# Optimization experiments

Hardware: AMD Instinct MI355X
Metric: run time of the kernel (lower is better)

The kernel has to match this reference:

```python
import jax, jax.numpy as jnp
import numpy as np


def _rel_shift(x):
    # Transformer-XL relative shift. x: [batch, heads, qlen, klen]
    b, n, i, j = x.shape
    x = jnp.pad(x, ((0, 0), (0, 0), (0, 0), (1, 0)))  # zero-pad along key axis
    x = x.reshape(b, n, j + 1, i)[:, :, 1:, :]
    return x.reshape(b, n, i, j)


def setup_inputs() -> dict:
    key = jax.random.key(0)
    ks = jax.random.split(key, 7)
    QLEN, B, D, H, DH = 2048, 4, 1024, 16, 64
    DO = H * DH
    s = 1.0 / np.sqrt(D)
    return {
        "word_embed": jax.random.normal(ks[0], (QLEN, B, D), jnp.float32),
        "pos_embed": jax.random.normal(ks[1], (QLEN, D), jnp.float32),
        "bias_q": jax.random.normal(ks[2], (H, DH), jnp.float32) * 0.02,
        "bias_k": jax.random.normal(ks[3], (H, DH), jnp.float32) * 0.02,
        "W_qkv": jax.random.normal(ks[4], (D, 3 * DO), jnp.float32) * s,
        "W_r": jax.random.normal(ks[5], (D, DO), jnp.float32) * s,
        "b_r": jnp.zeros((DO,), jnp.float32),
    }


def reference(word_embed, pos_embed, bias_q, bias_k, W_qkv, W_r, b_r):
    qlen, bsz, dim = word_embed.shape
    H, Dh = bias_q.shape
    plen = pos_embed.shape[0]

    # fused QKV projection (no bias, as in torch Linear(bias=False))
    qkv = jnp.einsum('ibd,de->ibe', word_embed, W_qkv)  # [qlen, b, 3*H*Dh]
    q, k, v = jnp.split(qkv, 3, axis=-1)
    q = q.reshape(qlen, bsz, H, Dh)
    k = k.reshape(qlen, bsz, H, Dh)
    v = v.reshape(qlen, bsz, H, Dh)

    # positional projection (r_net has bias)
    r = (pos_embed @ W_r + b_r).reshape(plen, H, Dh)  # [plen, H, Dh]

    # content (AC) and position (BD) score terms
    AC = jnp.einsum('ibnd,jbnd->bnij', q + bias_q, k)   # [b, H, qlen, klen]
    BD = jnp.einsum('ibnd,jnd->bnij', q + bias_k, r)    # [b, H, qlen, plen]
    BD = _rel_shift(BD)

    scale = float(Dh) ** 0.5
    attn = jax.nn.softmax((AC + BD) / scale, axis=-1)
    ctx = jnp.einsum('bnij,jbnd->ibnd', attn, v)        # [qlen, b, H, Dh]
    return ctx.reshape(qlen, bsz, H * Dh)
```

## Files before the change

kernel.cpp:

```cpp
#include <hip/hip_runtime.h>
#include <stdint.h>

typedef unsigned short u16;
typedef __attribute__((ext_vector_type(8))) short  s16x8;
typedef __attribute__((ext_vector_type(8))) __bf16 b16x8;
typedef __attribute__((ext_vector_type(4))) float  f32x4;

__device__ __forceinline__ float bf2f(u16 u){
  union { unsigned int ui; float f; } v; v.ui = ((unsigned int)u) << 16; return v.f;
}
__device__ __forceinline__ u16 f2bf(float f){
  union { float f; unsigned int ui; } v; v.f = f;
  unsigned int u = v.ui;
  u += 0x7FFFu + ((u >> 16) & 1u);
  return (u16)(u >> 16);
}
__device__ __forceinline__ f32x4 mfma16(s16x8 a, s16x8 b, f32x4 c){
  return __builtin_amdgcn_mfma_f32_16x16x32_bf16(
      __builtin_bit_cast(b16x8, a), __builtin_bit_cast(b16x8, b), c, 0, 0, 0);
}
__device__ __forceinline__ void gload_lds16(const u16* g, u16* l){
  __builtin_amdgcn_global_load_lds(
      (const __attribute__((address_space(1))) unsigned int*)(g),
      (__attribute__((address_space(3))) unsigned int*)(l), 16, 0, 0);
}

__global__ __launch_bounds__(256) void cast_f32_bf16(const float* __restrict__ in,
                                                     u16* __restrict__ out, int n8){
  int i = blockIdx.x * 256 + threadIdx.x;
  if (i >= n8) return;
  const f32x4* p = (const f32x4*)(in + (size_t)i * 8);
  f32x4 a = p[0], c = p[1];
  s16x8 o;
#pragma unroll
  for (int j = 0; j < 4; j++){ o[j] = (short)f2bf(a[j]); o[j+4] = (short)f2bf(c[j]); }
  *(s16x8*)(out + (size_t)i * 8) = o;
}

__global__ __launch_bounds__(256) void tcast(const float* __restrict__ in,
                                             u16* __restrict__ out, int R, int C){
  __shared__ float tile[32][33];
  int c0 = blockIdx.x * 32, r0 = blockIdx.y * 32;
  int tc = threadIdx.x & 31, tr = threadIdx.x >> 5;
#pragma unroll
  for (int p = 0; p < 4; p++)
    tile[tr + 8*p][tc] = in[(size_t)(r0 + tr + 8*p) * C + c0 + tc];
  __syncthreads();
  int rr = threadIdx.x & 31, cc = threadIdx.x >> 5;
#pragma unroll
  for (int p = 0; p < 4; p++)
    out[(size_t)(c0 + cc + 8*p) * R + r0 + rr] = f2bf(tile[rr][cc + 8*p]);
}

__global__ __launch_bounds__(256) void gemm_bt(const u16* __restrict__ A,
                                               const u16* __restrict__ Bt,
                                               int mode,
                                               u16* __restrict__ Qo, u16* __restrict__ Ko,
                                               u16* __restrict__ Vo, u16* __restrict__ Ro,
                                               const float* __restrict__ brp){
  __shared__ __align__(16) u16 lsA[2][128 * 32];
  __shared__ __align__(16) u16 lsB[2][128 * 32];
  int m0 = blockIdx.y * 128, n0 = blockIdx.x * 128;
  int t = threadIdx.x, wid = t >> 6, lane = t & 63;
  int lrow = lane & 15, lk = lane >> 4;
  int wr = wid >> 1, wc = wid & 1;

  f32x4 acc[4][4];
#pragma unroll
  for (int i = 0; i < 4; i++)
#pragma unroll
    for (int j = 0; j < 4; j++) acc[i][j] = (f32x4){0.f, 0.f, 0.f, 0.f};

  const u16* Ab = A  + (size_t)m0 * 1024;
  const u16* Bb = Bt + (size_t)n0 * 1024;

  s16x8 ra[2], rb[2];
#pragma unroll
  for (int p = 0; p < 2; p++){
    int c = p * 256 + t;
    ra[p] = *(const s16x8*)(Ab + (size_t)(c >> 2) * 1024 + (c & 3) * 8);
    rb[p] = *(const s16x8*)(Bb + (size_t)(c >> 2) * 1024 + (c & 3) * 8);
  }

  for (int kt = 0; kt < 32; kt++){
    int buf = kt & 1;
#pragma unroll
    for (int p = 0; p < 2; p++){
      int c = p * 256 + t;
      *(s16x8*)(lsA[buf] + (size_t)c * 8) = ra[p];
      *(s16x8*)(lsB[buf] + (size_t)c * 8) = rb[p];
    }
    __syncthreads();
    if (kt < 31){
      int k0 = (kt + 1) * 32;
#pragma unroll
      for (int p = 0; p < 2; p++){
        int c = p * 256 + t;
        ra[p] = *(const s16x8*)(Ab + (size_t)(c >> 2) * 1024 + k0 + (c & 3) * 8);
        rb[p] = *(const s16x8*)(Bb + (size_t)(c >> 2) * 1024 + k0 + (c & 3) * 8);
      }
    }
    s16x8 af[4], bfr[4];
#pragma unroll
    for (int i = 0; i < 4; i++)
      af[i] = *(const s16x8*)(lsA[buf] + (wr * 64 + i * 16 + lrow) * 32 + lk * 8);
#pragma unroll
    for (int j = 0; j < 4; j++)
      bfr[j] = *(const s16x8*)(lsB[buf] + (wc * 64 + j * 16 + lrow) * 32 + lk * 8);
#pragma unroll
    for (int i = 0; i < 4; i++)
#pragma unroll
      for (int j = 0; j < 4; j++)
        acc[i][j] = mfma16(af[i], bfr[j], acc[i][j]);
    __syncthreads();
  }

#pragma unroll
  for (int i = 0; i < 4; i++)
#pragma unroll
    for (int j = 0; j < 4; j++){
      int mbase = m0 + wr * 64 + i * 16 + lk * 4;
      int ncol  = n0 + wc * 64 + j * 16 + lrow;
#pragma unroll
      for (int r = 0; r < 4; r++){
        int m = mbase + r;
        float val = acc[i][j][r];
        if (mode == 0){
          int sel = ncol >> 10;
          int hd = ncol & 1023;
          int h = hd >> 6, dh = hd & 63;
          int b = m & 3, iq = m >> 2;
          size_t o = ((size_t)(b * 16 + h) * 2048 + iq) * 64 + dh;
          u16 vb = f2bf(val);
          if (sel == 0) Qo[o] = vb; else if (sel == 1) Ko[o] = vb; else Vo[o] = vb;
        } else {
          int h = ncol >> 6, dh = ncol & 63;
          Ro[((size_t)h * 2048 + m) * 64 + dh] = f2bf(val + brp[ncol]);
        }
      }
    }
}

__global__ __launch_bounds__(256) void transpose_v(const u16* __restrict__ V,
                                                   u16* __restrict__ VT){
  __shared__ u16 tile[64][65];
  int bh = blockIdx.y, i0 = blockIdx.x * 64;
  const u16* src = V + ((size_t)bh * 2048 + i0) * 64;
  int t = threadIdx.x;
#pragma unroll
  for (int p = 0; p < 2; p++){
    int idx = (p * 256 + t) * 8;
    int row = idx >> 6, col = idx & 63;
    s16x8 v = *(const s16x8*)(src + idx);
#pragma unroll
    for (int e = 0; e < 8; e++) tile[row][col + e] = (u16)v[e];
  }
  __syncthreads();
  u16* dst = VT + (size_t)bh * 64 * 2048 + i0;
#pragma unroll
  for (int p = 0; p < 2; p++){
    int idx = (p * 256 + t) * 8;
    int dh = idx >> 6, ii = idx & 63;
    s16x8 o;
#pragma unroll
    for (int e = 0; e < 8; e++) o[e] = (short)tile[ii + e][dh];
    *(s16x8*)(dst + (size_t)dh * 2048 + ii) = o;
  }
}

__global__ __launch_bounds__(256) void attn3_kernel(const u16* __restrict__ Qm,
                                                    const u16* __restrict__ Km,
                                                    const u16* __restrict__ Vt,
                                                    const u16* __restrict__ Rm,
                                                    const float* __restrict__ bq,
                                                    const float* __restrict__ bk,
                                                    float* __restrict__ Out){
  __shared__ __align__(16) u16   Kt[2][64 * 64];
  __shared__ __align__(16) u16   Vs[2][64 * 64];
  __shared__ __align__(16) float Gs[4][16 * 84];

  int lin = blockIdx.x;
  int xcd = lin & 7, j = lin >> 3;
  int hb = xcd * 8 + (j >> 5);
  int bx = j & 31;
  int h = hb & 15, b = hb >> 4;

  const int wid = threadIdx.x >> 6, lane = threadIdx.x & 63;
  const int lrow = lane & 15, lk = lane >> 4;
  const int q0 = bx * 64 + wid * 16;
  const size_t bh = (size_t)b * 16 + h;
  const u16* Qp = Qm + bh * 2048 * 64;
  const u16* Kp = Km + bh * 2048 * 64;
  const u16* Vp = Vt + bh * 64 * 2048;
  const u16* Rp = Rm + (size_t)h * 2048 * 64;
  float* Gw = Gs[wid];
  u16*   Pw = (u16*)Gs[wid];

  s16x8 qa[2], qb0[2], qb1[2];
  {
    const float* bqp = bq + h * 64;
    const float* bkp = bk + h * 64;
    int r1 = q0 + lrow + 1; if (r1 > 2047) r1 = 2047;
#pragma unroll
    for (int d = 0; d < 2; d++){
      int doff = d * 32 + lk * 8;
      s16x8 raw  = *(const s16x8*)(Qp + (size_t)(q0 + lrow) * 64 + doff);
      s16x8 raw1 = *(const s16x8*)(Qp + (size_t)r1 * 64 + doff);
      s16x8 a, c0, c1;
#pragma unroll
      for (int jj = 0; jj < 8; jj++){
        float qv = bf2f((u16)raw[jj]);
        float q1 = bf2f((u16)raw1[jj]);
        a[jj]  = (short)f2bf(qv + bqp[doff + jj]);
        c0[jj] = (short)f2bf(qv + bkp[doff + jj]);
        c1[jj] = (short)f2bf(q1 + bkp[doff + jj]);
      }
      qa[d] = a; qb0[d] = c0; qb1[d] = c1;
    }
  }

  float m = -3.0e38f, l = 0.f;
  f32x4 Oc[4];
#pragma unroll
  for (int f = 0; f < 4; f++) Oc[f] = (f32x4){0.f, 0.f, 0.f, 0.f};

  const float cs = 0.125f * 1.44269504088896f;
  const int wbase = 15 - lrow + 4 * lk;

  {
#pragma unroll
    for (int i = 0; i < 2; i++){
      int g = wid * 2 + i;
      int row = g * 8 + (lane >> 3);
      int sch = (lane & 7) ^ (row & 7);
      gload_lds16(Kp + (size_t)row * 64 + sch * 8, Kt[0] + g * 512);
      gload_lds16(Vp + (size_t)row * 2048 + 0 + sch * 8, Vs[0] + g * 512);
    }
  }
  __syncthreads();

  for (int t = 0; t < 32; t++){
    const int k0 = t * 64;
    const int cur = t & 1;
    const int d0 = k0 - q0;
    const bool n1 = (d0 <= 15);
    const bool n2 = (d0 >= -61);

    const int pb1 = n1 ? (d0 + 2032) : (d0 - 17);
    s16x8 rr[5][2];
#pragma unroll
    for (int wf = 0; wf < 5; wf++){
      int pr = pb1 + wf * 16 + lrow;
      pr = pr < 0 ? 0 : (pr > 2047 ? 2047 : pr);
#pragma unroll
      for (int d = 0; d < 2; d++)
        rr[wf][d] = *(const s16x8*)(Rp + (size_t)pr * 64 + d * 32 + lk * 8);
    }

    if (t < 31){
      const u16* Kn = Kp + (size_t)(k0 + 64) * 64;
#pragma unroll
      for (int i = 0; i < 2; i++){
        int g = wid * 2 + i;
        int row = g * 8 + (lane >> 3);
        int sch = (lane & 7) ^ (row & 7);
        gload_lds16(Kn + (size_t)row * 64 + sch * 8, Kt[cur ^ 1] + g * 512);
        gload_lds16(Vp + (size_t)row * 2048 + (k0 + 64) + sch * 8, Vs[cur ^ 1] + g * 512);
      }
    }

    f32x4 S[4];
#pragma unroll
    for (int kf = 0; kf < 4; kf++){
      f32x4 acc = (f32x4){0.f, 0.f, 0.f, 0.f};
#pragma unroll
      for (int d = 0; d < 2; d++){
        int row = kf * 16 + lrow;
        int ch = (d * 4 + lk) ^ (row & 7);
        s16x8 kfr = *(const s16x8*)(Kt[cur] + row * 64 + ch * 8);
        acc = mfma16(kfr, qa[d], acc);
      }
      S[kf] = acc;
    }

    const int dlane = d0 + 4 * lk - lrow;

    {
      const s16x8* qs = n1 ? qb0 : qb1;
#pragma unroll
      for (int wf = 0; wf < 5; wf++){
        f32x4 g = (f32x4){0.f, 0.f, 0.f, 0.f};
#pragma unroll
        for (int d = 0; d < 2; d++) g = mfma16(rr[wf][d], qs[d], g);
        *(f32x4*)(Gw + lrow * 84 + wf * 16 + 4 * lk) = g;
      }
      const float* gp = Gw + lrow * 84 + wbase;
      if (n1){
#pragma unroll
        for (int kf = 0; kf < 4; kf++)
#pragma unroll
          for (int r = 0; r < 4; r++){
            float g = gp[kf * 16 + r];
            S[kf][r] += (dlane + kf * 16 + r <= 0) ? g : 0.f;
          }
      } else {
#pragma unroll
        for (int kf = 0; kf < 4; kf++)
#pragma unroll
          for (int r = 0; r < 4; r++){
            float g = gp[kf * 16 + r];
            S[kf][r] += (dlane + kf * 16 + r >= 2) ? g : 0.f;
          }
      }
    }
    if (n1 && n2){
      const int pb2 = d0 - 17;
#pragma unroll
      for (int wf = 0; wf < 5; wf++){
        int pr = pb2 + wf * 16 + lrow;
        pr = pr < 0 ? 0 : (pr > 2047 ? 2047 : pr);
#pragma unroll
        for (int d = 0; d < 2; d++)
          rr[wf][d] = *(const s16x8*)(Rp + (size_t)pr * 64 + d * 32 + lk * 8);
      }
#pragma unroll
      for (int wf = 0; wf < 5; wf++){
        f32x4 g = (f32x4){0.f, 0.f, 0.f, 0.f};
#pragma unroll
        for (int d = 0; d < 2; d++) g = mfma16(rr[wf][d], qb1[d], g);
        *(f32x4*)(Gw + lrow * 84 + wf * 16 + 4 * lk) = g;
      }
      const float* gp = Gw + lrow * 84 + wbase;
#pragma unroll
      for (int kf = 0; kf < 4; kf++)
#pragma unroll
        for (int r = 0; r < 4; r++){
          float g = gp[kf * 16 + r];
          S[kf][r] += (dlane + kf * 16 + r >= 2) ? g : 0.f;
        }
    }

    float tmax = -3.0e38f;
#pragma unroll
    for (int kf = 0; kf < 4; kf++)
#pragma unroll
      for (int r = 0; r < 4; r++){
        float s = S[kf][r] * cs;
        S[kf][r] = s;
        tmax = fmaxf(tmax, s);
      }
    tmax = fmaxf(tmax, __shfl_xor(tmax, 16, 64));
    tmax = fmaxf(tmax, __shfl_xor(tmax, 32, 64));
    if (tmax > m + 11.5f){
      float al = exp2f(m - tmax);
      l *= al;
#pragma unroll
      for (int f = 0; f < 4; f++) Oc[f] *= al;
      m = tmax;
    }
    float sum = 0.f;
#pragma unroll
    for (int kf = 0; kf < 4; kf++)
#pragma unroll
      for (int r = 0; r < 4; r++){
        float p = exp2f(S[kf][r] - m);
        S[kf][r] = p;
        sum += p;
      }
    sum += __shfl_xor(sum, 16, 64);
    sum += __shfl_xor(sum, 32, 64);
    l += sum;

#pragma unroll
    for (int kf = 0; kf < 4; kf++)
#pragma unroll
      for (int m2 = 0; m2 < 2; m2++){
        uint32_t u = (uint32_t)f2bf(S[kf][2 * m2]) |
                     ((uint32_t)f2bf(S[kf][2 * m2 + 1]) << 16);
        *(uint32_t*)(Pw + lrow * 88 + kf * 16 + 4 * lk + 2 * m2) = u;
      }
#pragma unroll
    for (int ks = 0; ks < 2; ks++){
      s16x8 pB = *(const s16x8*)(Pw + lrow * 88 + ks * 32 + lk * 8);
#pragma unroll
      for (int f = 0; f < 4; f++){
        int row = f * 16 + lrow;
        int ch = (ks * 4 + lk) ^ (row & 7);
        s16x8 vfr = *(const s16x8*)(Vs[cur] + row * 64 + ch * 8);
        Oc[f] = mfma16(vfr, pB, Oc[f]);
      }
    }
    __syncthreads();
  }

  float inv = 1.0f / l;
#pragma unroll
  for (int f = 0; f < 4; f++){
    f32x4 o = Oc[f] * inv;
    *(f32x4*)(Out + (size_t)(q0 + lrow) * 4096 + b * 1024 + h * 64 + f * 16 + 4 * lk) = o;
  }
}

extern "C" void kernel_launch(void* const* d_in, const int* in_sizes, int n_in,
                              void* d_out, int out_size, void* d_ws, size_t ws_size,
                              hipStream_t stream){
  const float* word = (const float*)d_in[0];
  const float* pos  = (const float*)d_in[1];
  const float* bq   = (const float*)d_in[2];
  const float* bk   = (const float*)d_in[3];
  const float* Wqkv = (const float*)d_in[4];
  const float* Wr   = (const float*)d_in[5];
  const float* br   = (const float*)d_in[6];
  float* out = (float*)d_out;

  char* ws = (char*)d_ws;
  size_t off = 0;
  u16* Abf   = (u16*)(ws + off); off += (size_t)8192 * 1024 * 2;
  u16* WqkvT = (u16*)(ws + off); off += (size_t)3072 * 1024 * 2;
  u16* Pbf   = (u16*)(ws + off); off += (size_t)2048 * 1024 * 2;
  u16* WrT   = (u16*)(ws + off); off += (size_t)1024 * 1024 * 2;
  u16* Qb    = (u16*)(ws + off); off += (size_t)64 * 2048 * 64 * 2;
  u16* Kb    = (u16*)(ws + off); off += (size_t)64 * 2048 * 64 * 2;
  u16* Vb    = (u16*)(ws + off); off += (size_t)64 * 2048 * 64 * 2;
  u16* VTb   = (u16*)(ws + off); off += (size_t)64 * 64 * 2048 * 2;
  u16* Rb    = (u16*)(ws + off); off += (size_t)16 * 2048 * 64 * 2;
  if (ws_size < off) return;

  cast_f32_bf16<<<4096, 256, 0, stream>>>(word, Abf, 1048576);
  cast_f32_bf16<<<1024, 256, 0, stream>>>(pos,  Pbf, 262144);
  tcast<<<dim3(96, 32), 256, 0, stream>>>(Wqkv, WqkvT, 1024, 3072);
  tcast<<<dim3(32, 32), 256, 0, stream>>>(Wr,   WrT,   1024, 1024);
  gemm_bt<<<dim3(24, 64), 256, 0, stream>>>(Abf, WqkvT, 0, Qb, Kb, Vb, nullptr, nullptr);
  gemm_bt<<<dim3(8, 16),  256, 0, stream>>>(Pbf, WrT,   1, nullptr, nullptr, nullptr, Rb, br);
  transpose_v<<<dim3(32, 64), 256, 0, stream>>>(Vb, VTb);
  attn3_kernel<<<2048, 256, 0, stream>>>(Qb, Kb, VTb, Rb, bq, bk, out);
}
```

Before: 548.9 us.

## Write V transposed from GEMM, pad R buffer, stream V from registers in attention

The QKV GEMM epilogue now writes V directly in transposed layout, which removes the separate transpose kernel and the intermediate V buffer. R is stored in a padded per-head buffer so the attention kernel can step linear pointers without clamping. V tiles are loaded from global memory straight into registers instead of staged through LDS, and the softmax scale is folded into the biased Q. The change also adds packed bf16 conversion, setprio around MFMA sections and a launch-bounds occupancy hint. The transposed V stores in the GEMM epilogue are strided and uncoalesced, and the padded rows of R are never written, so their contents are left unset.

```diff
diff --git a/kernel.cpp b/kernel.cpp
--- a/kernel.cpp
+++ b/kernel.cpp
@@ -23,6 +23,11 @@
   __builtin_amdgcn_global_load_lds(
       (const __attribute__((address_space(1))) unsigned int*)(g),
       (__attribute__((address_space(3))) unsigned int*)(l), 16, 0, 0);
+}
+__device__ __forceinline__ uint32_t cvt_pk_bf16(float lo, float hi){
+  uint32_t r;
+  asm("v_cvt_pk_bf16_f32 %0, %1, %2" : "=v"(r) : "v"(lo), "v"(hi));
+  return r;
 }
 
 __global__ __launch_bounds__(256) void cast_f32_bf16(const float* __restrict__ in,
@@ -56,7 +61,7 @@
                                                const u16* __restrict__ Bt,
                                                int mode,
                                                u16* __restrict__ Qo, u16* __restrict__ Ko,
-                                               u16* __restrict__ Vo, u16* __restrict__ Ro,
+                                               u16* __restrict__ VTo, u16* __restrict__ Ro,
                                                const float* __restrict__ brp){
   __shared__ __align__(16) u16 lsA[2][128 * 32];
   __shared__ __align__(16) u16 lsB[2][128 * 32];
@@ -130,53 +135,61 @@
           int hd = ncol & 1023;
           int h = hd >> 6, dh = hd & 63;
           int b = m & 3, iq = m >> 2;
-          size_t o = ((size_t)(b * 16 + h) * 2048 + iq) * 64 + dh;
           u16 vb = f2bf(val);
-          if (sel == 0) Qo[o] = vb; else if (sel == 1) Ko[o] = vb; else Vo[o] = vb;
+          if (sel == 0)      Qo[((size_t)(b * 16 + h) * 2048 + iq) * 64 + dh] = vb;
+          else if (sel == 1) Ko[((size_t)(b * 16 + h) * 2048 + iq) * 64 + dh] = vb;
+          else               VTo[((size_t)(b * 16 + h) * 64 + dh) * 2048 + iq] = vb;
         } else {
           int h = ncol >> 6, dh = ncol & 63;
-          Ro[((size_t)h * 2048 + m) * 64 + dh] = f2bf(val + brp[ncol]);
+          Ro[((size_t)h * 4224 + m) * 64 + dh] = f2bf(val + brp[ncol]);
         }
       }
     }
 }
 
-__global__ __launch_bounds__(256) void transpose_v(const u16* __restrict__ V,
-                                                   u16* __restrict__ VT){
-  __shared__ u16 tile[64][65];
-  int bh = blockIdx.y, i0 = blockIdx.x * 64;
-  const u16* src = V + ((size_t)bh * 2048 + i0) * 64;
-  int t = threadIdx.x;
-#pragma unroll
-  for (int p = 0; p < 2; p++){
-    int idx = (p * 256 + t) * 8;
-    int row = idx >> 6, col = idx & 63;
-    s16x8 v = *(const s16x8*)(src + idx);
-#pragma unroll
-    for (int e = 0; e < 8; e++) tile[row][col + e] = (u16)v[e];
-  }
-  __syncthreads();
-  u16* dst = VT + (size_t)bh * 64 * 2048 + i0;
-#pragma unroll
-  for (int p = 0; p < 2; p++){
-    int idx = (p * 256 + t) * 8;
-    int dh = idx >> 6, ii = idx & 63;
-    s16x8 o;
-#pragma unroll
-    for (int e = 0; e < 8; e++) o[e] = (short)tile[ii + e][dh];
-    *(s16x8*)(dst + (size_t)dh * 2048 + ii) = o;
-  }
-}
-
-__global__ __launch_bounds__(256) void attn3_kernel(const u16* __restrict__ Qm,
-                                                    const u16* __restrict__ Km,
-                                                    const u16* __restrict__ Vt,
-                                                    const u16* __restrict__ Rm,
-                                                    const float* __restrict__ bq,
-                                                    const float* __restrict__ bk,
-                                                    float* __restrict__ Out){
+__device__ __forceinline__ void bd_pass(const u16* rp, const s16x8* qs, float* Gw,
+                                        int lrow, int lk){
+  s16x8 ra[2][2];
+  ra[0][0] = *(const s16x8*)(rp);
+  ra[0][1] = *(const s16x8*)(rp + 32);
+  ra[1][0] = *(const s16x8*)(rp + 1024);
+  ra[1][1] = *(const s16x8*)(rp + 1024 + 32);
+#pragma unroll
+  for (int wf = 0; wf < 5; wf++){
+    s16x8 c0 = ra[wf & 1][0], c1 = ra[wf & 1][1];
+    if (wf < 3){
+      ra[wf & 1][0] = *(const s16x8*)(rp + (wf + 2) * 1024);
+      ra[wf & 1][1] = *(const s16x8*)(rp + (wf + 2) * 1024 + 32);
+    }
+    f32x4 g = (f32x4){0.f, 0.f, 0.f, 0.f};
+    g = mfma16(c0, qs[0], g);
+    g = mfma16(c1, qs[1], g);
+    *(f32x4*)(Gw + lrow * 84 + wf * 16 + 4 * lk) = g;
+  }
+}
+template<bool GE2>
+__device__ __forceinline__ void bd_gather(const float* Gw, f32x4* S,
+                                          int lrow, int lk, int dlane, int wbase){
+  const float* gp = Gw + lrow * 84 + wbase;
+#pragma unroll
+  for (int kf = 0; kf < 4; kf++)
+#pragma unroll
+    for (int r = 0; r < 4; r++){
+      float g = gp[kf * 16 + r];
+      int dl = dlane + kf * 16 + r;
+      bool sel = GE2 ? (dl >= 2) : (dl <= 0);
+      S[kf][r] += sel ? g : 0.f;
+    }
+}
+
+__global__ __launch_bounds__(256, 4) void attn4_kernel(const u16* __restrict__ Qm,
+                                                       const u16* __restrict__ Km,
+                                                       const u16* __restrict__ Vt,
+                                                       const u16* __restrict__ Rm,
+                                                       const float* __restrict__ bq,
+                                                       const float* __restrict__ bk,
+                                                       float* __restrict__ Out){
   __shared__ __align__(16) u16   Kt[2][64 * 64];
-  __shared__ __align__(16) u16   Vs[2][64 * 64];
   __shared__ __align__(16) float Gs[4][16 * 84];
 
   int lin = blockIdx.x;
@@ -192,9 +205,11 @@
   const u16* Qp = Qm + bh * 2048 * 64;
   const u16* Kp = Km + bh * 2048 * 64;
   const u16* Vp = Vt + bh * 64 * 2048;
-  const u16* Rp = Rm + (size_t)h * 2048 * 64;
+  const u16* Rp = Rm + ((size_t)h * 4224 + 128) * 64;
   float* Gw = Gs[wid];
   u16*   Pw = (u16*)Gs[wid];
+
+  const float cs = 0.125f * 1.44269504088896f;
 
   s16x8 qa[2], qb0[2], qb1[2];
   {
@@ -211,31 +226,32 @@
       for (int jj = 0; jj < 8; jj++){
         float qv = bf2f((u16)raw[jj]);
         float q1 = bf2f((u16)raw1[jj]);
-        a[jj]  = (short)f2bf(qv + bqp[doff + jj]);
-        c0[jj] = (short)f2bf(qv + bkp[doff + jj]);
-        c1[jj] = (short)f2bf(q1 + bkp[doff + jj]);
+        a[jj]  = (short)f2bf(cs * (qv + bqp[doff + jj]));
+        c0[jj] = (short)f2bf(cs * (qv + bkp[doff + jj]));
+        c1[jj] = (short)f2bf(cs * (q1 + bkp[doff + jj]));
       }
       qa[d] = a; qb0[d] = c0; qb1[d] = c1;
     }
   }
+
+  const u16* r1p = Rp + (size_t)(2032 - q0 + lrow) * 64 + lk * 8;
+  const u16* r2p = r1p - (size_t)2049 * 64;
+  const u16* vp0 = Vp + (size_t)lrow * 2048 + lk * 8;
 
   float m = -3.0e38f, l = 0.f;
   f32x4 Oc[4];
 #pragma unroll
   for (int f = 0; f < 4; f++) Oc[f] = (f32x4){0.f, 0.f, 0.f, 0.f};
 
-  const float cs = 0.125f * 1.44269504088896f;
   const int wbase = 15 - lrow + 4 * lk;
-
-  {
-#pragma unroll
-    for (int i = 0; i < 2; i++){
-      int g = wid * 2 + i;
-      int row = g * 8 + (lane >> 3);
-      int sch = (lane & 7) ^ (row & 7);
-      gload_lds16(Kp + (size_t)row * 64 + sch * 8, Kt[0] + g * 512);
-      gload_lds16(Vp + (size_t)row * 2048 + 0 + sch * 8, Vs[0] + g * 512);
-    }
+  const int dl0   = 4 * lk - lrow;
+
+#pragma unroll
+  for (int i = 0; i < 2; i++){
+    int g = wid * 2 + i;
+    int row = g * 8 + (lane >> 3);
+    int sch = (lane & 7) ^ (row & 7);
+    gload_lds16(Kp + (size_t)row * 64 + sch * 8, Kt[0] + g * 512);
   }
   __syncthreads();
 
@@ -246,16 +262,10 @@
     const bool n1 = (d0 <= 15);
     const bool n2 = (d0 >= -61);
 
-    const int pb1 = n1 ? (d0 + 2032) : (d0 - 17);
-    s16x8 rr[5][2];
-#pragma unroll
-    for (int wf = 0; wf < 5; wf++){
-      int pr = pb1 + wf * 16 + lrow;
-      pr = pr < 0 ? 0 : (pr > 2047 ? 2047 : pr);
-#pragma unroll
-      for (int d = 0; d < 2; d++)
-        rr[wf][d] = *(const s16x8*)(Rp + (size_t)pr * 64 + d * 32 + lk * 8);
-    }
+    s16x8 v0[4];
+#pragma unroll
+    for (int f = 0; f < 4; f++)
+      v0[f] = *(const s16x8*)(vp0 + (size_t)f * 16 * 2048 + k0);
 
     if (t < 31){
       const u16* Kn = Kp + (size_t)(k0 + 64) * 64;
@@ -265,11 +275,11 @@
         int row = g * 8 + (lane >> 3);
         int sch = (lane & 7) ^ (row & 7);
         gload_lds16(Kn + (size_t)row * 64 + sch * 8, Kt[cur ^ 1] + g * 512);
-        gload_lds16(Vp + (size_t)row * 2048 + (k0 + 64) + sch * 8, Vs[cur ^ 1] + g * 512);
       }
     }
 
     f32x4 S[4];
+    __builtin_amdgcn_s_setprio(1);
 #pragma unroll
     for (int kf = 0; kf < 4; kf++){
       f32x4 acc = (f32x4){0.f, 0.f, 0.f, 0.f};
@@ -282,73 +292,30 @@
       }
       S[kf] = acc;
     }
-
-    const int dlane = d0 + 4 * lk - lrow;
-
-    {
-      const s16x8* qs = n1 ? qb0 : qb1;
-#pragma unroll
-      for (int wf = 0; wf < 5; wf++){
-        f32x4 g = (f32x4){0.f, 0.f, 0.f, 0.f};
-#pragma unroll
-        for (int d = 0; d < 2; d++) g = mfma16(rr[wf][d], qs[d], g);
-        *(f32x4*)(Gw + lrow * 84 + wf * 16 + 4 * lk) = g;
-      }
-      const float* gp = Gw + lrow * 84 + wbase;
-      if (n1){
-#pragma unroll
-        for (int kf = 0; kf < 4; kf++)
-#pragma unroll
-          for (int r = 0; r < 4; r++){
-            float g = gp[kf * 16 + r];
-            S[kf][r] += (dlane + kf * 16 + r <= 0) ? g : 0.f;
-          }
-      } else {
-#pragma unroll
-        for (int kf = 0; kf < 4; kf++)
-#pragma unroll
-          for (int r = 0; r < 4; r++){
-            float g = gp[kf * 16 + r];
-            S[kf][r] += (dlane + kf * 16 + r >= 2) ? g : 0.f;
-          }
-      }
-    }
-    if (n1 && n2){
-      const int pb2 = d0 - 17;
-#pragma unroll
-      for (int wf = 0; wf < 5; wf++){
-        int pr = pb2 + wf * 16 + lrow;
-        pr = pr < 0 ? 0 : (pr > 2047 ? 2047 : pr);
-#pragma unroll
-        for (int d = 0; d < 2; d++)
-          rr[wf][d] = *(const s16x8*)(Rp + (size_t)pr * 64 + d * 32 + lk * 8);
-      }
-#pragma unroll
-      for (int wf = 0; wf < 5; wf++){
-        f32x4 g = (f32x4){0.f, 0.f, 0.f, 0.f};
-#pragma unroll
-        for (int d = 0; d < 2; d++) g = mfma16(rr[wf][d], qb1[d], g);
-        *(f32x4*)(Gw + lrow * 84 + wf * 16 + 4 * lk) = g;
-      }
-      const float* gp = Gw + lrow * 84 + wbase;
-#pragma unroll
-      for (int kf = 0; kf < 4; kf++)
-#pragma unroll
-        for (int r = 0; r < 4; r++){
-          float g = gp[kf * 16 + r];
-          S[kf][r] += (dlane + kf * 16 + r >= 2) ? g : 0.f;
-        }
-    }
+    __builtin_amdgcn_s_setprio(0);
+
+    if (n1){
+      bd_pass(r1p, qb0, Gw, lrow, lk);
+      bd_gather<false>(Gw, S, lrow, lk, d0 + dl0, wbase);
+      if (n2){
+        bd_pass(r2p, qb1, Gw, lrow, lk);
+        bd_gather<true>(Gw, S, lrow, lk, d0 + dl0, wbase);
+      }
+    } else {
+      bd_pass(r2p, qb1, Gw, lrow, lk);
+      bd_gather<true>(Gw, S, lrow, lk, d0 + dl0, wbase);
+    }
+
+    s16x8 v1[4];
+#pragma unroll
+    for (int f = 0; f < 4; f++)
+      v1[f] = *(const s16x8*)(vp0 + (size_t)f * 16 * 2048 + k0 + 32);
 
     float tmax = -3.0e38f;
 #pragma unroll
     for (int kf = 0; kf < 4; kf++)
 #pragma unroll
-      for (int r = 0; r < 4; r++){
-        float s = S[kf][r] * cs;
-        S[kf][r] = s;
-        tmax = fmaxf(tmax, s);
-      }
+      for (int r = 0; r < 4; r++) tmax = fmaxf(tmax, S[kf][r]);
     tmax = fmaxf(tmax, __shfl_xor(tmax, 16, 64));
     tmax = fmaxf(tmax, __shfl_xor(tmax, 32, 64));
     if (tmax > m + 11.5f){
@@ -372,24 +339,25 @@
     l += sum;
 
 #pragma unroll
-    for (int kf = 0; kf < 4; kf++)
-#pragma unroll
-      for (int m2 = 0; m2 < 2; m2++){
-        uint32_t u = (uint32_t)f2bf(S[kf][2 * m2]) |
-                     ((uint32_t)f2bf(S[kf][2 * m2 + 1]) << 16);
-        *(uint32_t*)(Pw + lrow * 88 + kf * 16 + 4 * lk + 2 * m2) = u;
-      }
-#pragma unroll
-    for (int ks = 0; ks < 2; ks++){
-      s16x8 pB = *(const s16x8*)(Pw + lrow * 88 + ks * 32 + lk * 8);
-#pragma unroll
-      for (int f = 0; f < 4; f++){
-        int row = f * 16 + lrow;
-        int ch = (ks * 4 + lk) ^ (row & 7);
-        s16x8 vfr = *(const s16x8*)(Vs[cur] + row * 64 + ch * 8);
-        Oc[f] = mfma16(vfr, pB, Oc[f]);
-      }
-    }
+    for (int kf = 0; kf < 4; kf++){
+      uint32_t u0 = cvt_pk_bf16(S[kf][0], S[kf][1]);
+      uint32_t u1 = cvt_pk_bf16(S[kf][2], S[kf][3]);
+      *(uint32_t*)(Pw + lrow * 88 + kf * 16 + 4 * lk)     = u0;
+      *(uint32_t*)(Pw + lrow * 88 + kf * 16 + 4 * lk + 2) = u1;
+    }
+
+    __builtin_amdgcn_s_setprio(1);
+    {
+      s16x8 pB0 = *(const s16x8*)(Pw + lrow * 88 + lk * 8);
+#pragma unroll
+      for (int f = 0; f < 4; f++) Oc[f] = mfma16(v0[f], pB0, Oc[f]);
+      s16x8 pB1 = *(const s16x8*)(Pw + lrow * 88 + 32 + lk * 8);
+#pragma unroll
+      for (int f = 0; f < 4; f++) Oc[f] = mfma16(v1[f], pB1, Oc[f]);
+    }
+    __builtin_amdgcn_s_setprio(0);
+
+    r1p += 64 * 64; r2p += 64 * 64;
     __syncthreads();
   }
 
@@ -421,17 +389,16 @@
   u16* WrT   = (u16*)(ws + off); off += (size_t)1024 * 1024 * 2;
   u16* Qb    = (u16*)(ws + off); off += (size_t)64 * 2048 * 64 * 2;
   u16* Kb    = (u16*)(ws + off); off += (size_t)64 * 2048 * 64 * 2;
-  u16* Vb    = (u16*)(ws + off); off += (size_t)64 * 2048 * 64 * 2;
   u16* VTb   = (u16*)(ws + off); off += (size_t)64 * 64 * 2048 * 2;
-  u16* Rb    = (u16*)(ws + off); off += (size_t)16 * 2048 * 64 * 2;
+  u16* Rb    = (u16*)(ws + off); off += (size_t)16 * 4224 * 64 * 2;
   if (ws_size < off) return;
 
   cast_f32_bf16<<<4096, 256, 0, stream>>>(word, Abf, 1048576);
   cast_f32_bf16<<<1024, 256, 0, stream>>>(pos,  Pbf, 262144);
   tcast<<<dim3(96, 32), 256, 0, stream>>>(Wqkv, WqkvT, 1024, 3072);
   tcast<<<dim3(32, 32), 256, 0, stream>>>(Wr,   WrT,   1024, 1024);
-  gemm_bt<<<dim3(24, 64), 256, 0, stream>>>(Abf, WqkvT, 0, Qb, Kb, Vb, nullptr, nullptr);
-  gemm_bt<<<dim3(8, 16),  256, 0, stream>>>(Pbf, WrT,   1, nullptr, nullptr, nullptr, Rb, br);
-  transpose_v<<<dim3(32, 64), 256, 0, stream>>>(Vb, VTb);
-  attn3_kernel<<<2048, 256, 0, stream>>>(Qb, Kb, VTb, Rb, bq, bk, out);
-}
+  gemm_bt<<<dim3(24, 64), 256, 0, stream>>>(Abf, WqkvT, 0, Qb, Kb, VTb, nullptr, nullptr);
+  gemm_bt<<<dim3(8, 16),  256, 0, stream>>>(Pbf, WrT, 1, nullptr, nullptr, nullptr,
+                                            Rb + (size_t)128 * 64, br);
+  attn4_kernel<<<2048, 256, 0, stream>>>(Qb, Kb, VTb, Rb, bq, bk, out);
+}
```

After: 689.8 us. 25.7% more time.

## Load V directly to registers, pad R to drop clamps, fold scale into Q

Applied to the files above, without the earlier changes.

Removes the LDS staging buffer for V, so each wave loads V fragments straight from global memory into registers, and drops one LDS buffer to raise occupancy (launch bounds 3). R is stored in a padded buffer with guard rows, so relative-position loads use plain pointer increments instead of clamped index math. The softmax scale is folded into the biased Q fragments. It also adds a packed bf16 convert instruction and s_setprio around the MFMA sections. The risks are more global-load latency in the inner loop and uninitialized padding rows that are read and then masked.

```diff
diff --git a/kernel.cpp b/kernel.cpp
--- a/kernel.cpp
+++ b/kernel.cpp
@@ -23,6 +23,11 @@
   __builtin_amdgcn_global_load_lds(
       (const __attribute__((address_space(1))) unsigned int*)(g),
       (__attribute__((address_space(3))) unsigned int*)(l), 16, 0, 0);
+}
+__device__ __forceinline__ uint32_t cvt_pk_bf16(float lo, float hi){
+  uint32_t r;
+  asm("v_cvt_pk_bf16_f32 %0, %1, %2" : "=v"(r) : "v"(lo), "v"(hi));
+  return r;
 }
 
 __global__ __launch_bounds__(256) void cast_f32_bf16(const float* __restrict__ in,
@@ -135,7 +140,7 @@
           if (sel == 0) Qo[o] = vb; else if (sel == 1) Ko[o] = vb; else Vo[o] = vb;
         } else {
           int h = ncol >> 6, dh = ncol & 63;
-          Ro[((size_t)h * 2048 + m) * 64 + dh] = f2bf(val + brp[ncol]);
+          Ro[((size_t)h * 4224 + m) * 64 + dh] = f2bf(val + brp[ncol]);
         }
       }
     }
@@ -168,15 +173,14 @@
   }
 }
 
-__global__ __launch_bounds__(256) void attn3_kernel(const u16* __restrict__ Qm,
-                                                    const u16* __restrict__ Km,
-                                                    const u16* __restrict__ Vt,
-                                                    const u16* __restrict__ Rm,
-                                                    const float* __restrict__ bq,
-                                                    const float* __restrict__ bk,
-                                                    float* __restrict__ Out){
+__global__ __launch_bounds__(256, 3) void attn8_kernel(const u16* __restrict__ Qm,
+                                                       const u16* __restrict__ Km,
+                                                       const u16* __restrict__ Vt,
+                                                       const u16* __restrict__ Rm,
+                                                       const float* __restrict__ bq,
+                                                       const float* __restrict__ bk,
+                                                       float* __restrict__ Out){
   __shared__ __align__(16) u16   Kt[2][64 * 64];
-  __shared__ __align__(16) u16   Vs[2][64 * 64];
   __shared__ __align__(16) float Gs[4][16 * 84];
 
   int lin = blockIdx.x;
@@ -192,9 +196,11 @@
   const u16* Qp = Qm + bh * 2048 * 64;
   const u16* Kp = Km + bh * 2048 * 64;
   const u16* Vp = Vt + bh * 64 * 2048;
-  const u16* Rp = Rm + (size_t)h * 2048 * 64;
+  const u16* Rp = Rm + ((size_t)h * 4224 + 128) * 64;
   float* Gw = Gs[wid];
   u16*   Pw = (u16*)Gs[wid];
+
+  const float cs = 0.125f * 1.44269504088896f;
 
   s16x8 qa[2], qb0[2], qb1[2];
   {
@@ -211,31 +217,32 @@
       for (int jj = 0; jj < 8; jj++){
         float qv = bf2f((u16)raw[jj]);
         float q1 = bf2f((u16)raw1[jj]);
-        a[jj]  = (short)f2bf(qv + bqp[doff + jj]);
-        c0[jj] = (short)f2bf(qv + bkp[doff + jj]);
-        c1[jj] = (short)f2bf(q1 + bkp[doff + jj]);
+        a[jj]  = (short)f2bf(cs * (qv + bqp[doff + jj]));
+        c0[jj] = (short)f2bf(cs * (qv + bkp[doff + jj]));
+        c1[jj] = (short)f2bf(cs * (q1 + bkp[doff + jj]));
       }
       qa[d] = a; qb0[d] = c0; qb1[d] = c1;
     }
   }
+
+  const u16* r1p = Rp + (size_t)(2032 - q0 + lrow) * 64 + lk * 8;
+  const u16* r2p = r1p - (size_t)2049 * 64;
+  const u16* vp0 = Vp + (size_t)lrow * 2048 + lk * 8;
 
   float m = -3.0e38f, l = 0.f;
   f32x4 Oc[4];
 #pragma unroll
   for (int f = 0; f < 4; f++) Oc[f] = (f32x4){0.f, 0.f, 0.f, 0.f};
 
-  const float cs = 0.125f * 1.44269504088896f;
   const int wbase = 15 - lrow + 4 * lk;
-
-  {
-#pragma unroll
-    for (int i = 0; i < 2; i++){
-      int g = wid * 2 + i;
-      int row = g * 8 + (lane >> 3);
-      int sch = (lane & 7) ^ (row & 7);
-      gload_lds16(Kp + (size_t)row * 64 + sch * 8, Kt[0] + g * 512);
-      gload_lds16(Vp + (size_t)row * 2048 + 0 + sch * 8, Vs[0] + g * 512);
-    }
+  const int dl0   = 4 * lk - lrow;
+
+#pragma unroll
+  for (int i = 0; i < 2; i++){
+    int g = wid * 2 + i;
+    int row = g * 8 + (lane >> 3);
+    int sch = (lane & 7) ^ (row & 7);
+    gload_lds16(Kp + (size_t)row * 64 + sch * 8, Kt[0] + g * 512);
   }
   __syncthreads();
 
@@ -245,16 +252,14 @@
     const int d0 = k0 - q0;
     const bool n1 = (d0 <= 15);
     const bool n2 = (d0 >= -61);
-
-    const int pb1 = n1 ? (d0 + 2032) : (d0 - 17);
+    const int dlane = d0 + dl0;
+
+    const u16* rp = n1 ? r1p : r2p;
     s16x8 rr[5][2];
 #pragma unroll
     for (int wf = 0; wf < 5; wf++){
-      int pr = pb1 + wf * 16 + lrow;
-      pr = pr < 0 ? 0 : (pr > 2047 ? 2047 : pr);
-#pragma unroll
-      for (int d = 0; d < 2; d++)
-        rr[wf][d] = *(const s16x8*)(Rp + (size_t)pr * 64 + d * 32 + lk * 8);
+      rr[wf][0] = *(const s16x8*)(rp + wf * 1024);
+      rr[wf][1] = *(const s16x8*)(rp + wf * 1024 + 32);
     }
 
     if (t < 31){
@@ -265,11 +270,16 @@
         int row = g * 8 + (lane >> 3);
         int sch = (lane & 7) ^ (row & 7);
         gload_lds16(Kn + (size_t)row * 64 + sch * 8, Kt[cur ^ 1] + g * 512);
-        gload_lds16(Vp + (size_t)row * 2048 + (k0 + 64) + sch * 8, Vs[cur ^ 1] + g * 512);
-      }
-    }
+      }
+    }
+
+    s16x8 v0[4];
+#pragma unroll
+    for (int f = 0; f < 4; f++)
+      v0[f] = *(const s16x8*)(vp0 + (size_t)f * 16 * 2048 + k0);
 
     f32x4 S[4];
+    __builtin_amdgcn_s_setprio(1);
 #pragma unroll
     for (int kf = 0; kf < 4; kf++){
       f32x4 acc = (f32x4){0.f, 0.f, 0.f, 0.f};
@@ -282,16 +292,15 @@
       }
       S[kf] = acc;
     }
-
-    const int dlane = d0 + 4 * lk - lrow;
+    __builtin_amdgcn_s_setprio(0);
 
     {
       const s16x8* qs = n1 ? qb0 : qb1;
 #pragma unroll
       for (int wf = 0; wf < 5; wf++){
         f32x4 g = (f32x4){0.f, 0.f, 0.f, 0.f};
-#pragma unroll
-        for (int d = 0; d < 2; d++) g = mfma16(rr[wf][d], qs[d], g);
+        g = mfma16(rr[wf][0], qs[0], g);
+        g = mfma16(rr[wf][1], qs[1], g);
         *(f32x4*)(Gw + lrow * 84 + wf * 16 + 4 * lk) = g;
       }
       const float* gp = Gw + lrow * 84 + wbase;
@@ -314,20 +323,16 @@
       }
     }
     if (n1 && n2){
-      const int pb2 = d0 - 17;
 #pragma unroll
       for (int wf = 0; wf < 5; wf++){
-        int pr = pb2 + wf * 16 + lrow;
-        pr = pr < 0 ? 0 : (pr > 2047 ? 2047 : pr);
-#pragma unroll
-        for (int d = 0; d < 2; d++)
-          rr[wf][d] = *(const s16x8*)(Rp + (size_t)pr * 64 + d * 32 + lk * 8);
+        rr[wf][0] = *(const s16x8*)(r2p + wf * 1024);
+        rr[wf][1] = *(const s16x8*)(r2p + wf * 1024 + 32);
       }
 #pragma unroll
       for (int wf = 0; wf < 5; wf++){
         f32x4 g = (f32x4){0.f, 0.f, 0.f, 0.f};
-#pragma unroll
-        for (int d = 0; d < 2; d++) g = mfma16(rr[wf][d], qb1[d], g);
+        g = mfma16(rr[wf][0], qb1[0], g);
+        g = mfma16(rr[wf][1], qb1[1], g);
         *(f32x4*)(Gw + lrow * 84 + wf * 16 + 4 * lk) = g;
       }
       const float* gp = Gw + lrow * 84 + wbase;
@@ -340,15 +345,16 @@
         }
     }
 
+    s16x8 v1[4];
+#pragma unroll
+    for (int f = 0; f < 4; f++)
+      v1[f] = *(const s16x8*)(vp0 + (size_t)f * 16 * 2048 + k0 + 32);
+
     float tmax = -3.0e38f;
 #pragma unroll
     for (int kf = 0; kf < 4; kf++)
 #pragma unroll
-      for (int r = 0; r < 4; r++){
-        float s = S[kf][r] * cs;
-        S[kf][r] = s;
-        tmax = fmaxf(tmax, s);
-      }
+      for (int r = 0; r < 4; r++) tmax = fmaxf(tmax, S[kf][r]);
     tmax = fmaxf(tmax, __shfl_xor(tmax, 16, 64));
     tmax = fmaxf(tmax, __shfl_xor(tmax, 32, 64));
     if (tmax > m + 11.5f){
@@ -372,24 +378,25 @@
     l += sum;
 
 #pragma unroll
-    for (int kf = 0; kf < 4; kf++)
-#pragma unroll
-      for (int m2 = 0; m2 < 2; m2++){
-        uint32_t u = (uint32_t)f2bf(S[kf][2 * m2]) |
-                     ((uint32_t)f2bf(S[kf][2 * m2 + 1]) << 16);
-        *(uint32_t*)(Pw + lrow * 88 + kf * 16 + 4 * lk + 2 * m2) = u;
-      }
-#pragma unroll
-    for (int ks = 0; ks < 2; ks++){
-      s16x8 pB = *(const s16x8*)(Pw + lrow * 88 + ks * 32 + lk * 8);
-#pragma unroll
-      for (int f = 0; f < 4; f++){
-        int row = f * 16 + lrow;
-        int ch = (ks * 4 + lk) ^ (row & 7);
-        s16x8 vfr = *(const s16x8*)(Vs[cur] + row * 64 + ch * 8);
-        Oc[f] = mfma16(vfr, pB, Oc[f]);
-      }
-    }
+    for (int kf = 0; kf < 4; kf++){
+      uint32_t u0 = cvt_pk_bf16(S[kf][0], S[kf][1]);
+      uint32_t u1 = cvt_pk_bf16(S[kf][2], S[kf][3]);
+      *(uint32_t*)(Pw + lrow * 88 + kf * 16 + 4 * lk)     = u0;
+      *(uint32_t*)(Pw + lrow * 88 + kf * 16 + 4 * lk + 2) = u1;
+    }
+
+    __builtin_amdgcn_s_setprio(1);
+    {
+      s16x8 pB0 = *(const s16x8*)(Pw + lrow * 88 + lk * 8);
+#pragma unroll
+      for (int f = 0; f < 4; f++) Oc[f] = mfma16(v0[f], pB0, Oc[f]);
+      s16x8 pB1 = *(const s16x8*)(Pw + lrow * 88 + 32 + lk * 8);
+#pragma unroll
+      for (int f = 0; f < 4; f++) Oc[f] = mfma16(v1[f], pB1, Oc[f]);
+    }
+    __builtin_amdgcn_s_setprio(0);
+
+    r1p += 64 * 64; r2p += 64 * 64;
     __syncthreads();
   }
 
@@ -423,7 +430,7 @@
   u16* Kb    = (u16*)(ws + off); off += (size_t)64 * 2048 * 64 * 2;
   u16* Vb    = (u16*)(ws + off); off += (size_t)64 * 2048 * 64 * 2;
   u16* VTb   = (u16*)(ws + off); off += (size_t)64 * 64 * 2048 * 2;
-  u16* Rb    = (u16*)(ws + off); off += (size_t)16 * 2048 * 64 * 2;
+  u16* Rb    = (u16*)(ws + off); off += (size_t)16 * 4224 * 64 * 2;
   if (ws_size < off) return;
 
   cast_f32_bf16<<<4096, 256, 0, stream>>>(word, Abf, 1048576);
@@ -431,7 +438,8 @@
   tcast<<<dim3(96, 32), 256, 0, stream>>>(Wqkv, WqkvT, 1024, 3072);
   tcast<<<dim3(32, 32), 256, 0, stream>>>(Wr,   WrT,   1024, 1024);
   gemm_bt<<<dim3(24, 64), 256, 0, stream>>>(Abf, WqkvT, 0, Qb, Kb, Vb, nullptr, nullptr);
-  gemm_bt<<<dim3(8, 16),  256, 0, stream>>>(Pbf, WrT,   1, nullptr, nullptr, nullptr, Rb, br);
+  gemm_bt<<<dim3(8, 16),  256, 0, stream>>>(Pbf, WrT, 1, nullptr, nullptr, nullptr,
+                                            Rb + (size_t)128 * 64, br);
   transpose_v<<<dim3(32, 64), 256, 0, stream>>>(Vb, VTb);
-  attn3_kernel<<<2048, 256, 0, stream>>>(Qb, Kb, VTb, Rb, bq, bk, out);
-}
+  attn8_kernel<<<2048, 256, 0, stream>>>(Qb, Kb, VTb, Rb, bq, bk, out);
+}
```

After: 665.4 us. 21.2% more time.
